# Optimization experiments

Hardware: AMD Instinct MI355X
Metric: run time of the kernel (lower is better)

Reference implementation:

```python
import jax, jax.numpy as jnp
import numpy as np
from jax import lax

WARMUP = 365
X1S = (100.0, 1200.0); X2S = (-5.0, 3.0); X3S = (20.0, 300.0); X4S = (1.1, 2.9)
K1, K2 = 3, 6  # max UH kernel lengths: ceil(x4_max)=3, ceil(2*x4_max)=6


def _uh_kernels(x4):
    # x4: [B]. S-curve differences, padded with zeros beyond ceil(x4)/ceil(2*x4).
    t1 = jnp.arange(K1 + 1, dtype=x4.dtype)
    sh1 = jnp.minimum(t1[None, :] / x4[:, None], 1.0) ** 2.5          # [B, K1+1]
    uh1 = sh1[:, 1:] - sh1[:, :-1]                                     # [B, K1]
    t2 = jnp.arange(K2 + 1, dtype=x4.dtype)
    r = t2[None, :] / x4[:, None]
    sh2 = jnp.where(t2[None, :] <= x4[:, None],
                    0.5 * r ** 2.5,
                    1.0 - 0.5 * jnp.maximum(2.0 - r, 0.0) ** 2.5)      # [B, K2+1]
    uh2 = sh2[:, 1:] - sh2[:, :-1]                                     # [B, K2]
    return uh1, uh2


def _causal_conv(x, uh):
    # x: [T, B], uh: [B, K] -> y[t,b] = sum_k uh[b,k] * x[t-k,b]
    T = x.shape[0]
    out = jnp.zeros_like(x)
    for k in range(uh.shape[1]):  # K is small and static (<=6)
        shifted = jnp.pad(x, ((k, 0), (0, 0)))[:T]
        out = out + uh[:, k][None, :] * shifted
    return out


def _gr4j_core(p_and_e, x1, x2, x3, x4, s0, r0):
    # p_and_e: [T, B, 2]
    diff = p_and_e[:, :, 0] - p_and_e[:, :, 1]
    pn = jnp.maximum(diff, 0.0)   # net precip [T, B]
    en = jnp.maximum(-diff, 0.0)  # net evap   [T, B]

    def prod_step(s, pe):
        p, e = pe
        s = jnp.clip(s, 0.0, x1)
        tp = jnp.tanh(p / x1)
        te = jnp.tanh(e / x1)
        ps = x1 * (1.0 - (s / x1) ** 2) * tp / (1.0 + s / x1 * tp)
        es = s * (2.0 - s / x1) * te / (1.0 + (1.0 - s / x1) * te)
        s2 = jnp.clip(s - es + ps, 0.0, x1)
        perc = s2 * (1.0 - (1.0 + (4.0 / 9.0 * s2 / x1) ** 4) ** (-0.25))
        s2 = s2 - perc
        pr = perc + (pn_step := p - ps) * 1.0 + 0.0 * pn_step  # pr = perc + (pn - ps)
        return s2, pr

    s_final, prs = lax.scan(prod_step, s0, (pn, en))  # prs: [T, B]

    uh1, uh2 = _uh_kernels(x4)
    q9 = _causal_conv(prs, uh1)  # [T, B]
    q1 = _causal_conv(prs, uh2)  # [T, B]

    def route_step(r, q):
        q9t, q1t = q
        r = jnp.clip(r, 0.0, x3)
        gex = x2 * (r / x3) ** 3.5
        r2 = jnp.maximum(0.0, r + q9t + gex)
        qr = r2 * (1.0 - (1.0 + (r2 / x3) ** 4) ** (-0.25))
        r2 = r2 - qr
        qd = jnp.maximum(0.0, q1t + gex)
        return r2, qr + qd

    r_final, q = lax.scan(route_step, r0, (q9, q1))  # q: [T, B]
    return q, s_final, r_final


def _forward(p_and_e, parameters):
    x1 = X1S[0] + parameters[:, 0] * (X1S[1] - X1S[0])
    x2 = X2S[0] + parameters[:, 1] * (X2S[1] - X2S[0])
    x3 = X3S[0] + parameters[:, 2] * (X3S[1] - X3S[0])
    x4 = X4S[0] + parameters[:, 3] * (X4S[1] - X4S[0])
    if WARMUP > 0:
        # warmup runs under no_grad in torch: stop gradients through it
        _, s_w, r_w = _gr4j_core(p_and_e[:WARMUP], x1, x2, x3, x4,
                                 0.5 * lax.stop_gradient(x1),
                                 0.5 * lax.stop_gradient(x3))
        s0 = lax.stop_gradient(s_w)
        r0 = lax.stop_gradient(r_w)
    else:
        s0 = 0.5 * lax.stop_gradient(x1)
        r0 = 0.5 * lax.stop_gradient(x3)
    q, _, _ = _gr4j_core(p_and_e[WARMUP:], x1, x2, x3, x4, s0, r0)
    return q[:, :, None]  # [T-WARMUP, B, 1]


def setup_inputs() -> dict:
    key = jax.random.key(0)
    k1, k2 = jax.random.split(key)
    p_and_e = jax.random.uniform(k1, (4015, 2048, 2), dtype=jnp.float32)
    parameters = jax.random.uniform(k2, (2048, 4), dtype=jnp.float32)
    return {"p_and_e": p_and_e, "parameters": parameters}


def reference(p_and_e, parameters):
    return _forward(p_and_e, parameters)
```

## Files before the change

### kernel.cpp

```cpp
#include <hip/hip_runtime.h>


#define T_TOTAL 4015
#define NWARM   365
#define NB      2048
#define BSTEP   55
#define NBATCH  73

__global__ __launch_bounds__(128, 1)
void gr4j_kernel(const float2* __restrict__ pe_in,
                 const float*  __restrict__ params,
                 float*        __restrict__ out)
{
    const int lane = threadIdx.x & 63;
    const int wid  = threadIdx.x >> 6;
    const int b    = blockIdx.x * 64 + lane;

    __shared__ float2 prbuf[2][BSTEP * 64];
    __shared__ int produced;
    __shared__ int consumed;
    if (threadIdx.x == 0) { produced = 0; consumed = 0; }
    __syncthreads();

    const float x1 = 100.0f + params[b * 4 + 0] * 1100.0f;
    const float x2 = -5.0f  + params[b * 4 + 1] * 8.0f;
    const float x3 = 20.0f  + params[b * 4 + 2] * 280.0f;
    const float x4 = 1.1f   + params[b * 4 + 3] * 1.8f;
    const float invx1 = __builtin_amdgcn_rcpf(x1);
    const float invx3 = __builtin_amdgcn_rcpf(x3);
    const float c49   = (4.0f / 9.0f) * invx1;
    const float c49_2 = c49 * c49;
    const float c4s   = c49_2 * c49_2;
    const float i3_2  = invx3 * invx3;
    const float c4r   = i3_2 * i3_2;

    if (wid == 0) {
        float u10, u11, u12, u20, u21, u22, u23, u24, u25;
        {
            float sh[3];
            #pragma unroll
            for (int j = 1; j <= 3; ++j)
                sh[j - 1] = powf(fminf((float)j / x4, 1.0f), 2.5f);
            u10 = sh[0]; u11 = sh[1] - sh[0]; u12 = sh[2] - sh[1];
            float s2h[6];
            #pragma unroll
            for (int j = 1; j <= 6; ++j) {
                float rr = (float)j / x4;
                s2h[j - 1] = ((float)j <= x4) ? 0.5f * powf(rr, 2.5f)
                           : 1.0f - 0.5f * powf(fmaxf(2.0f - rr, 0.0f), 2.5f);
            }
            u20 = s2h[0];          u21 = s2h[1] - s2h[0]; u22 = s2h[2] - s2h[1];
            u23 = s2h[3] - s2h[2]; u24 = s2h[4] - s2h[3]; u25 = s2h[5] - s2h[4];
        }

        float s = 0.5f * x1;
        float ph0 = 0.f, ph1 = 0.f, ph2 = 0.f, ph3 = 0.f, ph4 = 0.f;

        auto prod_step = [&](float2 pe) -> float2 {
            const float diff = pe.x - pe.y;
            const float pn = fmaxf(diff, 0.0f);
            const float en = fmaxf(-diff, 0.0f);
            const float ap = pn * invx1;
            const float ae = en * invx1;
            const float sx = s * invx1;
            const float dp = fmaf(sx, ap, 1.0f);
            const float de = fmaf(1.0f - sx, ae, 1.0f);
            const float n1 = fmaf(-sx, sx, 1.0f);
            const float nump = pn * n1;
            const float nume = (sx * en) * (2.0f - sx);
            const float dpde = dp * de;
            const float eps  = dpde - 1.0f;
            const float rpe  = fmaf(eps, eps - 1.0f, 1.0f);
            const float a_ = nump * de;
            const float b_ = nume * dp;
            const float s2 = fmaf(a_ - b_, rpe, s);
            const float ps = a_ * rpe;
            const float s22 = s2 * s2;
            const float s24 = s22 * s22;
            const float z = c4s * s24;
            float w = fmaf(z, 15.0f / 128.0f, -5.0f / 32.0f);
            w = fmaf(z, w, 0.25f);
            const float perc = (s2 * z) * w;
            s = s2 - perc;
            const float pr = perc + (pn - ps);
            const float q9 = fmaf(u10, pr, fmaf(u11, ph0, u12 * ph1));
            const float q1 = fmaf(u20, pr, fmaf(u21, ph0, fmaf(u22, ph1,
                             fmaf(u23, ph2, fmaf(u24, ph3, u25 * ph4)))));
            ph4 = ph3; ph3 = ph2; ph2 = ph1; ph1 = ph0; ph0 = pr;
            return make_float2(q9, q1);
        };

        const float2* gptr = pe_in + b;
        float2 rot[11];
        #pragma unroll
        for (int i = 0; i < 11; ++i) rot[i] = gptr[(size_t)i * NB];

        for (int k = 0; k < NBATCH; ++k) {
            if (k >= 2) {
                while (__hip_atomic_load(&consumed, __ATOMIC_ACQUIRE,
                                         __HIP_MEMORY_SCOPE_WORKGROUP) < k - 1) {}
            }
            float2* dst = &prbuf[k & 1][0] + lane;
            const int tb = k * BSTEP;
            if (k != 6) {
                const int grf = (k < NBATCH - 1) ? 5 : 4;
                for (int g = 0; g < 5; ++g) {
                    float2* d2 = dst + g * (11 * 64);
                    if (g < grf) {
                        const float2* gp = gptr + (size_t)(tb + g * 11 + 11) * NB;
                        #pragma unroll
                        for (int i = 0; i < 11; ++i) {
                            const float2 pe = rot[i];
                            rot[i] = gp[(size_t)i * NB];
                            d2[i * 64] = prod_step(pe);
                        }
                    } else {
                        #pragma unroll
                        for (int i = 0; i < 11; ++i)
                            d2[i * 64] = prod_step(rot[i]);
                    }
                }
            } else {
                const float2* gp = gptr + (size_t)(tb + 11) * NB;
                #pragma unroll
                for (int j = 0; j < 55; ++j) {
                    const int i = j % 11;
                    if (j == 35) { ph0 = ph1 = ph2 = ph3 = ph4 = 0.0f; }
                    const float2 pe = rot[i];
                    rot[i] = gp[(size_t)j * NB];
                    dst[j * 64] = prod_step(pe);
                }
            }
            __hip_atomic_store(&produced, k + 1, __ATOMIC_RELEASE,
                               __HIP_MEMORY_SCOPE_WORKGROUP);
        }
    } else {
        float r = 0.5f * x3;

        auto route_q = [&](float2 qq) -> float {
            const float q9 = qq.x, q1 = qq.y;
            float rx = fmaxf(r * invx3, 1e-12f);
            const float hx = 0.5f * rx;
            unsigned ib = __float_as_uint(rx);
            ib = 0x5f3759dfu - (ib >> 1);
            float t = __uint_as_float(ib);
            t = t * fmaf(-hx * t, t, 1.5f);
            t = t * fmaf(-hx * t, t, 1.5f);
            const float srx = rx * t;
            const float rx3 = (rx * rx) * rx;
            const float gex = (x2 * rx3) * srx;
            const float r2 = fmaxf(0.0f, (r + q9) + gex);
            const float r22 = r2 * r2;
            const float r24 = r22 * r22;
            const float xx = fmaf(c4r, r24, 1.0f);
            const float qx = 0.25f * xx;
            float y = fmaf(xx, fmaf(xx, 0.034855f, -0.26206f), 1.22721f);
            {
                const float y2 = y * y;
                const float y4 = y2 * y2;
                y = y * fmaf(-qx, y4, 1.25f);
            }
            {
                const float y2 = y * y;
                const float y4 = y2 * y2;
                y = y * fmaf(-qx, y4, 1.25f);
            }
            const float rn = r2 * y;
            const float qr = r2 - rn;
            r = rn;
            return qr + fmaxf(0.0f, q1 + gex);
        };

        for (int k = 0; k < NBATCH; ++k) {
            while (__hip_atomic_load(&produced, __ATOMIC_ACQUIRE,
                                     __HIP_MEMORY_SCOPE_WORKGROUP) < k + 1) {}
            const float2* src = &prbuf[k & 1][0] + lane;
            if (k != 6) {
                float* ob = (k < 6)
                    ? out + (size_t)(k * BSTEP) * NB + b
                    : out + (size_t)(k * BSTEP - NWARM) * NB + b;
                float2 prr[11];
                #pragma unroll
                for (int i = 0; i < 11; ++i) prr[i] = src[i * 64];
                for (int g = 0; g < 5; ++g) {
                    const float2* sp = src + (g + 1) * (11 * 64);
                    float* ob2 = ob + (size_t)(g * 11) * NB;
                    if (g < 4) {
                        #pragma unroll
                        for (int i = 0; i < 11; ++i) {
                            const float2 qq = prr[i];
                            prr[i] = sp[i * 64];
                            ob2[(size_t)i * NB] = route_q(qq);
                        }
                    } else {
                        #pragma unroll
                        for (int i = 0; i < 11; ++i)
                            ob2[(size_t)i * NB] = route_q(prr[i]);
                    }
                }
            } else {
                float* dumpb = out + (size_t)330 * NB + b;
                float* realb = out + b;
                float2 prr[11];
                #pragma unroll
                for (int i = 0; i < 11; ++i) prr[i] = src[i * 64];
                #pragma unroll
                for (int g = 0; g < 5; ++g) {
                    #pragma unroll
                    for (int i = 0; i < 11; ++i) {
                        const int j = g * 11 + i;
                        const float2 qq = prr[i];
                        if (g < 4) prr[i] = src[(j + 11) * 64];
                        const float q = route_q(qq);
                        if (j < 35) dumpb[(size_t)j * NB] = q;
                        else        realb[(size_t)(j - 35) * NB] = q;
                    }
                }
            }
            __hip_atomic_store(&consumed, k + 1, __ATOMIC_RELEASE,
                               __HIP_MEMORY_SCOPE_WORKGROUP);
        }
    }
}

extern "C" void kernel_launch(void* const* d_in, const int* in_sizes, int n_in,
                              void* d_out, int out_size, void* d_ws, size_t ws_size,
                              hipStream_t stream) {
    const float2* pe_in  = (const float2*)d_in[0];
    const float*  params = (const float*)d_in[1];
    float* out = (float*)d_out;
    (void)in_sizes; (void)n_in; (void)out_size; (void)d_ws; (void)ws_size;

    gr4j_kernel<<<dim3(NB / 64), dim3(128), 0, stream>>>(pe_in, params, out);
}
```

Before: 442.6 us.

## Normalize stores and replace routing root/power chain with Chebyshev polynomial fits

The production store is tracked as a normalized fraction, with the scale constants folded into the unit-hydrograph weights. The routing step now evaluates (1+u)^-0.25 and (1+u)^-0.875 through per-thread degree-15 Chebyshev fits, computed once at kernel start, in place of the Newton iterations and inverse square root. This shortens the serial dependency chain of the routing recurrence. In exchange it adds setup cost, raises register pressure from 32 coefficient registers, and relies on an assumed bound on the normalized routing store that may not hold for every input.

```diff
diff --git a/kernel.cpp b/kernel.cpp
--- a/kernel.cpp
+++ b/kernel.cpp
@@ -6,6 +6,46 @@
 #define NB      2048
 #define BSTEP   55
 #define NBATCH  73
+
+template<typename F>
+__device__ __attribute__((always_inline)) inline
+void cheb_fit15(F f, float (&a)[16]) {
+    float c[16];
+    #pragma unroll
+    for (int j = 0; j < 16; ++j) c[j] = 0.0f;
+    for (int k = 0; k < 32; ++k) {
+        const float th = 3.14159265358979f * ((float)k + 0.5f) / 32.0f;
+        const float t  = __builtin_cosf(th);
+        const float fv = f(t);
+        #pragma unroll
+        for (int j = 0; j < 16; ++j)
+            c[j] += fv * __builtin_cosf((float)j * th);
+    }
+    #pragma unroll
+    for (int j = 0; j < 16; ++j) c[j] *= (2.0f / 32.0f);
+    c[0] *= 0.5f;
+    float Tp[16], Tc[16];
+    #pragma unroll
+    for (int j = 0; j < 16; ++j) { Tp[j] = 0.0f; Tc[j] = 0.0f; a[j] = 0.0f; }
+    Tp[0] = 1.0f;
+    a[0] += c[0];
+    Tc[1] = 1.0f;
+    a[1] += c[1];
+    #pragma unroll
+    for (int j = 2; j < 16; ++j) {
+        float Tn[16];
+        #pragma unroll
+        for (int i = 0; i < 16; ++i) Tn[i] = -Tp[i];
+        #pragma unroll
+        for (int i = 1; i < 16; ++i) Tn[i] += 2.0f * Tc[i - 1];
+        #pragma unroll
+        for (int i = 0; i < 16; ++i) {
+            a[i] += c[j] * Tn[i];
+            Tp[i] = Tc[i];
+            Tc[i] = Tn[i];
+        }
+    }
+}
 
 __global__ __launch_bounds__(128, 1)
 void gr4j_kernel(const float2* __restrict__ pe_in,
@@ -28,20 +68,22 @@
     const float x4 = 1.1f   + params[b * 4 + 3] * 1.8f;
     const float invx1 = __builtin_amdgcn_rcpf(x1);
     const float invx3 = __builtin_amdgcn_rcpf(x3);
-    const float c49   = (4.0f / 9.0f) * invx1;
-    const float c49_2 = c49 * c49;
-    const float c4s   = c49_2 * c49_2;
-    const float i3_2  = invx3 * invx3;
-    const float c4r   = i3_2 * i3_2;
 
     if (wid == 0) {
-        float u10, u11, u12, u20, u21, u22, u23, u24, u25;
+        const float t49 = 4.0f / 9.0f;
+        const float cz  = (t49 * t49) * (t49 * t49);
+        const float AA  = 0.25f * cz;
+        const float BB  = -(5.0f / 32.0f) * cz * cz;
+        const float CC  = (15.0f / 128.0f) * cz * cz * cz;
+
+        float f10, f11, f12, g20, g21, g22, g23, g24, g25;
         {
             float sh[3];
             #pragma unroll
             for (int j = 1; j <= 3; ++j)
                 sh[j - 1] = powf(fminf((float)j / x4, 1.0f), 2.5f);
-            u10 = sh[0]; u11 = sh[1] - sh[0]; u12 = sh[2] - sh[1];
+            const float F = x1 * invx3;
+            f10 = sh[0] * F; f11 = (sh[1] - sh[0]) * F; f12 = (sh[2] - sh[1]) * F;
             float s2h[6];
             #pragma unroll
             for (int j = 1; j <= 6; ++j) {
@@ -49,11 +91,12 @@
                 s2h[j - 1] = ((float)j <= x4) ? 0.5f * powf(rr, 2.5f)
                            : 1.0f - 0.5f * powf(fmaxf(2.0f - rr, 0.0f), 2.5f);
             }
-            u20 = s2h[0];          u21 = s2h[1] - s2h[0]; u22 = s2h[2] - s2h[1];
-            u23 = s2h[3] - s2h[2]; u24 = s2h[4] - s2h[3]; u25 = s2h[5] - s2h[4];
-        }
-
-        float s = 0.5f * x1;
+            g20 = s2h[0] * x1;          g21 = (s2h[1] - s2h[0]) * x1;
+            g22 = (s2h[2] - s2h[1]) * x1; g23 = (s2h[3] - s2h[2]) * x1;
+            g24 = (s2h[4] - s2h[3]) * x1; g25 = (s2h[5] - s2h[4]) * x1;
+        }
+
+        float sg = 0.5f;
         float ph0 = 0.f, ph1 = 0.f, ph2 = 0.f, ph3 = 0.f, ph4 = 0.f;
 
         auto prod_step = [&](float2 pe) -> float2 {
@@ -62,32 +105,24 @@
             const float en = fmaxf(-diff, 0.0f);
             const float ap = pn * invx1;
             const float ae = en * invx1;
-            const float sx = s * invx1;
-            const float dp = fmaf(sx, ap, 1.0f);
-            const float de = fmaf(1.0f - sx, ae, 1.0f);
-            const float n1 = fmaf(-sx, sx, 1.0f);
-            const float nump = pn * n1;
-            const float nume = (sx * en) * (2.0f - sx);
-            const float dpde = dp * de;
-            const float eps  = dpde - 1.0f;
-            const float rpe  = fmaf(eps, eps - 1.0f, 1.0f);
-            const float a_ = nump * de;
-            const float b_ = nume * dp;
-            const float s2 = fmaf(a_ - b_, rpe, s);
-            const float ps = a_ * rpe;
+            const float oms = 1.0f - sg;
+            const float hp = sg * ap;
+            const float he = oms * ae;
+            const float psn = (ap * fmaf(-sg, sg, 1.0f)) * fmaf(hp, hp - 1.0f, 1.0f);
+            const float esn = ((sg * ae) * (2.0f - sg)) * fmaf(he, he - 1.0f, 1.0f);
+            const float s2  = (sg + psn) - esn;
             const float s22 = s2 * s2;
-            const float s24 = s22 * s22;
-            const float z = c4s * s24;
-            float w = fmaf(z, 15.0f / 128.0f, -5.0f / 32.0f);
-            w = fmaf(z, w, 0.25f);
-            const float perc = (s2 * z) * w;
-            s = s2 - perc;
-            const float pr = perc + (pn - ps);
-            const float q9 = fmaf(u10, pr, fmaf(u11, ph0, u12 * ph1));
-            const float q1 = fmaf(u20, pr, fmaf(u21, ph0, fmaf(u22, ph1,
-                             fmaf(u23, ph2, fmaf(u24, ph3, u25 * ph4)))));
-            ph4 = ph3; ph3 = ph2; ph2 = ph1; ph1 = ph0; ph0 = pr;
-            return make_float2(q9, q1);
+            const float zh  = s22 * s22;
+            const float w   = fmaf(fmaf(CC, zh, BB), zh, AA);
+            const float s2z = s2 * zh;
+            const float sn  = fmaf(-s2z, w, s2);
+            const float prn = (s2 - sn) + (ap - psn);
+            const float q9i = fmaf(f10, prn, fmaf(f11, ph0, f12 * ph1));
+            const float q1a = fmaf(g20, prn, fmaf(g21, ph0, fmaf(g22, ph1,
+                              fmaf(g23, ph2, fmaf(g24, ph3, g25 * ph4)))));
+            ph4 = ph3; ph3 = ph2; ph2 = ph1; ph1 = ph0; ph0 = prn;
+            sg = sn;
+            return make_float2(q9i, q1a);
         };
 
         const float2* gptr = pe_in + b;
@@ -135,40 +170,76 @@
                                __HIP_MEMORY_SCOPE_WORKGROUP);
         }
     } else {
-        float r = 0.5f * x3;
+        const float x2i = x2 * invx3;
+
+        float ah[16], ag[16];
+        float ku;
+        {
+            const float vm  = 1.02f + (4.1f + 0.0097f * x1) * invx3;
+            const float vm2 = vm * vm;
+            const float umax = vm2 * vm2;
+            ku = 2.0f / umax;
+            const float half_u = 0.5f * umax;
+            cheb_fit15([&](float t) {
+                const float u = half_u * (t + 1.0f);
+                return powf(1.0f + u, -0.25f);
+            }, ah);
+            cheb_fit15([&](float t) {
+                const float u = half_u * (t + 1.0f);
+                return powf(1.0f + u, -0.875f);
+            }, ag);
+        }
+
+        float rho = 0.5f;
+        float p35 = 0.08838835f;
 
         auto route_q = [&](float2 qq) -> float {
-            const float q9 = qq.x, q1 = qq.y;
-            float rx = fmaxf(r * invx3, 1e-12f);
-            const float hx = 0.5f * rx;
-            unsigned ib = __float_as_uint(rx);
-            ib = 0x5f3759dfu - (ib >> 1);
-            float t = __uint_as_float(ib);
-            t = t * fmaf(-hx * t, t, 1.5f);
-            t = t * fmaf(-hx * t, t, 1.5f);
-            const float srx = rx * t;
-            const float rx3 = (rx * rx) * rx;
-            const float gex = (x2 * rx3) * srx;
-            const float r2 = fmaxf(0.0f, (r + q9) + gex);
-            const float r22 = r2 * r2;
-            const float r24 = r22 * r22;
-            const float xx = fmaf(c4r, r24, 1.0f);
-            const float qx = 0.25f * xx;
-            float y = fmaf(xx, fmaf(xx, 0.034855f, -0.26206f), 1.22721f);
-            {
-                const float y2 = y * y;
-                const float y4 = y2 * y2;
-                y = y * fmaf(-qx, y4, 1.25f);
-            }
-            {
-                const float y2 = y * y;
-                const float y4 = y2 * y2;
-                y = y * fmaf(-qx, y4, 1.25f);
-            }
-            const float rn = r2 * y;
-            const float qr = r2 - rn;
-            r = rn;
-            return qr + fmaxf(0.0f, q1 + gex);
+            const float q9i = qq.x, q1a = qq.y;
+            const float v  = fmaf(x2i, p35, rho + q9i);
+            const float qd = fmaxf(0.0f, fmaf(x2, p35, q1a));
+            const float v2 = v * v;
+            const float u  = v2 * v2;
+            const float th = fminf(fmaf(ku, u, -1.0f), 1.0f);
+            const float th2 = th * th;
+            const float th4 = th2 * th2;
+            const float th8 = th4 * th4;
+            float b0 = fmaf(ah[1],  th, ah[0]);
+            float b1 = fmaf(ah[3],  th, ah[2]);
+            float b2 = fmaf(ah[5],  th, ah[4]);
+            float b3 = fmaf(ah[7],  th, ah[6]);
+            float b4 = fmaf(ah[9],  th, ah[8]);
+            float b5 = fmaf(ah[11], th, ah[10]);
+            float b6 = fmaf(ah[13], th, ah[12]);
+            float b7 = fmaf(ah[15], th, ah[14]);
+            float c0 = fmaf(b1, th2, b0);
+            float c1 = fmaf(b3, th2, b2);
+            float c2 = fmaf(b5, th2, b4);
+            float c3 = fmaf(b7, th2, b6);
+            float d0 = fmaf(c1, th4, c0);
+            float d1 = fmaf(c3, th4, c2);
+            const float H = fmaf(d1, th8, d0);
+            float e0 = fmaf(ag[1],  th, ag[0]);
+            float e1 = fmaf(ag[3],  th, ag[2]);
+            float e2 = fmaf(ag[5],  th, ag[4]);
+            float e3 = fmaf(ag[7],  th, ag[6]);
+            float e4 = fmaf(ag[9],  th, ag[8]);
+            float e5 = fmaf(ag[11], th, ag[10]);
+            float e6 = fmaf(ag[13], th, ag[12]);
+            float e7 = fmaf(ag[15], th, ag[14]);
+            float f0 = fmaf(e1, th2, e0);
+            float f1 = fmaf(e3, th2, e2);
+            float f2 = fmaf(e5, th2, e4);
+            float f3 = fmaf(e7, th2, e6);
+            float g0 = fmaf(f1, th4, f0);
+            float g1 = fmaf(f3, th4, f2);
+            const float H35 = fmaf(g1, th8, g0);
+            const float sv = __builtin_amdgcn_sqrtf(fmaxf(v, 0.0f));
+            const float v3 = v2 * v;
+            const float rn = v * H;
+            p35 = (v3 * sv) * H35;
+            const float q = fmaf(x3, v - rn, qd);
+            rho = rn;
+            return q;
         };
 
         for (int k = 0; k < NBATCH; ++k) {
```

Measured after the change: 514.6 us. +16.3%, slower.
